# Kernel optimization log

Measured on AMD Instinct MI355X. Metric: run time of the kernel, lower is better.

## Reference

```python
import jax, jax.numpy as jnp
import numpy as np

N, S, R, CM = 1, 128, 256, 256
C, CZ = 32, 128


def setup_inputs() -> dict:
    key = jax.random.key(0)
    k1, k2, k3, k4 = jax.random.split(key, 4)
    return {
        "msa_repr": jax.random.normal(k1, (N, S, R, CM), dtype=jnp.float32),
        "left_proj": jax.random.normal(k2, (CM, C), dtype=jnp.float32) * 0.05,
        "right_proj": jax.random.normal(k3, (CM, C), dtype=jnp.float32) * 0.05,
        "out_proj": jax.random.normal(k4, (C * C, CZ), dtype=jnp.float32) * 0.05,
    }


def reference(msa_repr, left_proj, right_proj, out_proj):
    # msa_repr: [N, S, R, CM]
    # Project to left/right activations and move R before S
    # (equivalent to torch matmul + transpose(-2, -3)).
    a = jnp.einsum("nsrm,mc->nrsc", msa_repr, left_proj)   # [N, R, S, C]
    b = jnp.einsum("nsrm,mc->nrsc", msa_repr, right_proj)  # [N, R, S, C]
    # Outer product contracted over the MSA dim S:
    # outer[n, r, t, c, e] = sum_s a[n, r, s, c] * b[n, t, s, e]
    outer = jnp.einsum("nrsc,ntse->nrtce", a, b)            # [N, R, R, C, C]
    n, r, t = outer.shape[:3]
    outer = outer.reshape(n, r, t, C * C)                   # [N, R, R, C*C]
    # Output projection to pair channels cz
    return outer @ out_proj                                 # [N, R, R, CZ]
```

## Files before the change

### kernel.cpp

```cpp
#include <hip/hip_runtime.h>

typedef __bf16 bf16x8 __attribute__((ext_vector_type(8)));
typedef __bf16 bf16x4 __attribute__((ext_vector_type(4)));
typedef float f32x16 __attribute__((ext_vector_type(16)));
typedef float f32x4 __attribute__((ext_vector_type(4)));

constexpr int S = 128, R = 256, CM = 256, C = 32, CZ = 128;

#define MFMA __builtin_amdgcn_mfma_f32_32x32x16_bf16

__device__ __forceinline__ bf16x4 cvt4(float a, float b, float c, float d) {
    bf16x4 r;
    r[0] = (__bf16)a; r[1] = (__bf16)b; r[2] = (__bf16)c; r[3] = (__bf16)d;
    return r;
}

__global__ __launch_bounds__(256) void k_prep(const float* __restrict__ W,
                                              const float* __restrict__ Lp,
                                              const float* __restrict__ Rp,
                                              __bf16* __restrict__ WTf,
                                              __bf16* __restrict__ WLRT) {
    int b = blockIdx.x;
    if (b < 512) {
        int g = b * 256 + threadIdx.x;
        int cz = g & 127;
        int k = g >> 7;
        int e = k >> 5, c = k & 31;
        float v = W[(size_t)(c * 32 + e) * 128 + cz];
        WTf[((size_t)(k >> 3) * 128 + cz) * 8 + (k & 7)] = (__bf16)v;
    } else {
        int c = b - 512;
        int m = threadIdx.x;
        const float* src = (c < 32) ? Lp : Rp;
        WLRT[(size_t)c * 256 + m] = (__bf16)src[(size_t)m * 32 + (c & 31)];
    }
}

__global__ __launch_bounds__(256) void k_proj(const float* __restrict__ msa,
                                              const __bf16* __restrict__ WLRT,
                                              __bf16* __restrict__ aTf,
                                              __bf16* __restrict__ bTf) {
    __shared__ __align__(16) __bf16 As[32 * 256];
    __shared__ __align__(16) char Pp[2 * 4096];
    const int r = blockIdx.x;
    const int sq = blockIdx.y;
    const int t = threadIdx.x;

#pragma unroll
    for (int it = 0; it < 8; ++it) {
        int idx = it * 256 + t;
        int row = idx >> 6;
        int cg = idx & 63;
        float4 v = *(const float4*)&msa[((size_t)(sq * 32 + row) * R + r) * CM + cg * 4];
        bf16x4 h = cvt4(v.x, v.y, v.z, v.w);
        int P = (cg >> 1) ^ (row & 15);
        *(bf16x4*)((char*)As + row * 512 + P * 16 + (cg & 1) * 8) = h;
    }
    __syncthreads();

    const int w = t >> 6;
    const int l = t & 63;
    const int l31 = t & 31;
    const int kh = (t >> 5) & 1;
    const int sd = w & 1;
    const int ksh = w >> 1;

    f32x16 acc;
#pragma unroll
    for (int q = 0; q < 16; ++q) acc[q] = 0.f;

    const bf16x8* wb = (const bf16x8*)&WLRT[(size_t)(sd * 32 + l31) * 256 + 8 * kh];
    const char* arow = (const char*)As + l31 * 512;

    __builtin_amdgcn_s_setprio(1);
#pragma unroll
    for (int j = 0; j < 8; ++j) {
        int ks = ksh * 8 + j;
        int P = (2 * ks + kh) ^ (l31 & 15);
        bf16x8 af = *(const bf16x8*)(arow + P * 16);
        acc = MFMA(af, wb[2 * ks], acc, 0, 0, 0);
    }
    __builtin_amdgcn_s_setprio(0);

    char* pbase = Pp + (size_t)sd * 4096;
    if (ksh == 1) {
#pragma unroll
        for (int pc = 0; pc < 4; ++pc) {
            f32x4 v;
            v[0] = acc[4 * pc + 0]; v[1] = acc[4 * pc + 1];
            v[2] = acc[4 * pc + 2]; v[3] = acc[4 * pc + 3];
            *(f32x4*)(pbase + ((pc * 64) + l) * 16) = v;
        }
    }
    __syncthreads();
    if (ksh == 0) {
#pragma unroll
        for (int pc = 0; pc < 4; ++pc) {
            f32x4 v = *(const f32x4*)(pbase + ((pc * 64) + l) * 16);
            acc[4 * pc + 0] += v[0]; acc[4 * pc + 1] += v[1];
            acc[4 * pc + 2] += v[2]; acc[4 * pc + 3] += v[3];
        }
        __bf16* dst = sd ? bTf : aTf;
#pragma unroll
        for (int q = 0; q < 4; ++q) {
            size_t base = (size_t)r * 4096 + (size_t)(2 * sq + (q >> 1)) * 512 +
                          (size_t)(q & 1) * 256 + (size_t)l31 * 8 + 4 * kh;
            *(bf16x4*)&dst[base] = cvt4(acc[4 * q + 0], acc[4 * q + 1],
                                        acc[4 * q + 2], acc[4 * q + 3]);
        }
    }
}

__global__ __launch_bounds__(512, 2) void k_main(const __bf16* __restrict__ aTf,
                                                 const __bf16* __restrict__ bTf,
                                                 const __bf16* __restrict__ WTf,
                                                 float* __restrict__ out) {
    __shared__ __align__(16) __bf16 Gs[64 * 1024];

    const int t = threadIdx.x;
    const int w = t >> 6;
    const int l = t & 63;
    const int lane = l & 31;
    const int kh = l >> 5;
    const int r0 = blockIdx.x * 8;
    const int t0 = blockIdx.y * 8;

    const int rg = w & 3;
    const int tg = w >> 2;

    f32x16 acc[2][4];
#pragma unroll
    for (int i = 0; i < 2; ++i)
#pragma unroll
        for (int j = 0; j < 4; ++j)
#pragma unroll
            for (int q = 0; q < 16; ++q) acc[i][j][q] = 0.f;

    const bf16x8* ap0 = (const bf16x8*)aTf + ((size_t)(r0 + 2 * rg + 0) * 512 + kh * 32 + lane);
    const bf16x8* ap1 = (const bf16x8*)aTf + ((size_t)(r0 + 2 * rg + 1) * 512 + kh * 32 + lane);
    const bf16x8* bp0 = (const bf16x8*)bTf + ((size_t)(t0 + 4 * tg + 0) * 512 + kh * 32 + lane);
    const bf16x8* bp1 = (const bf16x8*)bTf + ((size_t)(t0 + 4 * tg + 1) * 512 + kh * 32 + lane);
    const bf16x8* bp2 = (const bf16x8*)bTf + ((size_t)(t0 + 4 * tg + 2) * 512 + kh * 32 + lane);
    const bf16x8* bp3 = (const bf16x8*)bTf + ((size_t)(t0 + 4 * tg + 3) * 512 + kh * 32 + lane);

    bf16x8 Ap[3][2], Bp[3][4];
#pragma unroll
    for (int s = 0; s < 3; ++s) {
        Ap[s][0] = ap0[s * 64]; Ap[s][1] = ap1[s * 64];
        Bp[s][0] = bp0[s * 64]; Bp[s][1] = bp1[s * 64];
        Bp[s][2] = bp2[s * 64]; Bp[s][3] = bp3[s * 64];
    }
#pragma unroll
    for (int ks = 0; ks < 8; ++ks) {
        const int s = ks % 3;
        __builtin_amdgcn_s_setprio(1);
        acc[0][0] = MFMA(Ap[s][0], Bp[s][0], acc[0][0], 0, 0, 0);
        acc[0][1] = MFMA(Ap[s][0], Bp[s][1], acc[0][1], 0, 0, 0);
        acc[0][2] = MFMA(Ap[s][0], Bp[s][2], acc[0][2], 0, 0, 0);
        acc[0][3] = MFMA(Ap[s][0], Bp[s][3], acc[0][3], 0, 0, 0);
        acc[1][0] = MFMA(Ap[s][1], Bp[s][0], acc[1][0], 0, 0, 0);
        acc[1][1] = MFMA(Ap[s][1], Bp[s][1], acc[1][1], 0, 0, 0);
        acc[1][2] = MFMA(Ap[s][1], Bp[s][2], acc[1][2], 0, 0, 0);
        acc[1][3] = MFMA(Ap[s][1], Bp[s][3], acc[1][3], 0, 0, 0);
        __builtin_amdgcn_s_setprio(0);
        if (ks + 3 < 8) {
            const int kn = ks + 3;
            Ap[s][0] = ap0[kn * 64]; Ap[s][1] = ap1[kn * 64];
            Bp[s][0] = bp0[kn * 64]; Bp[s][1] = bp1[kn * 64];
            Bp[s][2] = bp2[kn * 64]; Bp[s][3] = bp3[kn * 64];
        }
    }

#pragma unroll
    for (int i = 0; i < 2; ++i) {
#pragma unroll
        for (int j = 0; j < 4; ++j) {
            int p = (2 * rg + i) * 8 + 4 * tg + j;
            unsigned prow = (unsigned)p * 2048;
#pragma unroll
            for (int q = 0; q < 4; ++q) {
                int Lc = lane * 4 + q;
                int P = Lc ^ (p & 15) ^ (lane & 7);
                *(bf16x4*)((char*)Gs + prow + (unsigned)P * 16 + kh * 8) =
                    cvt4(acc[i][j][4 * q + 0], acc[i][j][4 * q + 1],
                         acc[i][j][4 * q + 2], acc[i][j][4 * q + 3]);
            }
        }
    }
    __syncthreads();

    const int kq = w >> 1;
    const int ng = w & 1;
    const int czl0 = ng * 64 + lane;
    const int czl1 = czl0 + 32;
    const char* wb0c = (const char*)WTf + ((size_t)kh * 128 + czl0) * 16;
    const char* wb1c = (const char*)WTf + ((size_t)kh * 128 + czl1) * 16;
    const unsigned prow0 = (unsigned)lane * 2048;
    const unsigned prow1 = (unsigned)(lane + 32) * 2048;
    const int p15 = lane & 15;

    f32x16 o00, o01, o10, o11;
#pragma unroll
    for (int q = 0; q < 16; ++q) { o00[q] = 0.f; o01[q] = 0.f; o10[q] = 0.f; o11[q] = 0.f; }

    bf16x8 Wp[16][2];
#pragma unroll
    for (int s = 0; s < 16; ++s) {
        const char* a0 = wb0c + (size_t)(kq * 16 + s) * 4096;
        const char* a1 = wb1c + (size_t)(kq * 16 + s) * 4096;
        asm volatile("global_load_dwordx4 %0, %1, off" : "=v"(Wp[s][0]) : "v"(a0));
        asm volatile("global_load_dwordx4 %0, %1, off" : "=v"(Wp[s][1]) : "v"(a1));
    }

    bf16x8 Gp[4][2];
#define LDG(sl, kk) do { \
    int Lr = (kk) * 2 + kh; \
    int P = Lr ^ p15 ^ ((Lr >> 2) & 7); \
    Gp[sl][0] = *(const bf16x8*)((const char*)Gs + prow0 + (unsigned)P * 16); \
    Gp[sl][1] = *(const bf16x8*)((const char*)Gs + prow1 + (unsigned)P * 16); } while (0)

    LDG(0, kq * 16 + 0);
    LDG(1, kq * 16 + 1);
    LDG(2, kq * 16 + 2);
    LDG(3, kq * 16 + 3);

#define STEPB(j, cnt) do { \
    asm volatile("s_waitcnt vmcnt(" #cnt ")"); \
    __builtin_amdgcn_sched_barrier(0); \
    __builtin_amdgcn_s_setprio(1); \
    o00 = MFMA(Gp[(j) & 3][0], Wp[j][0], o00, 0, 0, 0); \
    o01 = MFMA(Gp[(j) & 3][0], Wp[j][1], o01, 0, 0, 0); \
    o10 = MFMA(Gp[(j) & 3][1], Wp[j][0], o10, 0, 0, 0); \
    o11 = MFMA(Gp[(j) & 3][1], Wp[j][1], o11, 0, 0, 0); \
    __builtin_amdgcn_s_setprio(0); \
    if ((j) + 4 < 16) LDG((j) & 3, kq * 16 + (j) + 4); \
} while (0)

    STEPB(0, 30);  STEPB(1, 28);  STEPB(2, 26);  STEPB(3, 24);
    STEPB(4, 22);  STEPB(5, 20);  STEPB(6, 18);  STEPB(7, 16);
    STEPB(8, 14);  STEPB(9, 12);  STEPB(10, 10); STEPB(11, 8);
    STEPB(12, 6);  STEPB(13, 4);  STEPB(14, 2);  STEPB(15, 0);

    __syncthreads();

    {
        char* pr = (char*)Gs + (size_t)w * 16384;
        const f32x16* os[4] = {&o00, &o01, &o10, &o11};
#pragma unroll
        for (int s2 = 0; s2 < 4; ++s2) {
#pragma unroll
            for (int pc = 0; pc < 4; ++pc) {
                f32x4 v;
                v[0] = (*os[s2])[4 * pc + 0]; v[1] = (*os[s2])[4 * pc + 1];
                v[2] = (*os[s2])[4 * pc + 2]; v[3] = (*os[s2])[4 * pc + 3];
                *(f32x4*)(pr + ((s2 * 4 + pc) * 64 + l) * 16) = v;
            }
        }
    }
    __syncthreads();

    {
        const int ngx = w >> 2;
        const int mix = (w >> 1) & 1;
        const int nix = w & 1;
        const int s2 = mix * 2 + nix;
        f32x16 sm;
#pragma unroll
        for (int q = 0; q < 16; ++q) sm[q] = 0.f;
#pragma unroll
        for (int kq2 = 0; kq2 < 4; ++kq2) {
            const char* pr = (const char*)Gs + (size_t)(kq2 * 2 + ngx) * 16384;
#pragma unroll
            for (int pc = 0; pc < 4; ++pc) {
                f32x4 v = *(const f32x4*)(pr + ((s2 * 4 + pc) * 64 + l) * 16);
                sm[4 * pc + 0] += v[0]; sm[4 * pc + 1] += v[1];
                sm[4 * pc + 2] += v[2]; sm[4 * pc + 3] += v[3];
            }
        }
        const int czl = ngx * 64 + nix * 32 + (l & 31);
        const int khx = l >> 5;
#pragma unroll
        for (int reg = 0; reg < 16; ++reg) {
            int pl = mix * 32 + (reg & 3) + 8 * (reg >> 2) + 4 * khx;
            int prr = pl >> 3, ptt = pl & 7;
            out[((size_t)(r0 + prr) * 256 + (t0 + ptt)) * 128 + czl] = sm[reg];
        }
    }
}

extern "C" void kernel_launch(void* const* d_in, const int* in_sizes, int n_in,
                              void* d_out, int out_size, void* d_ws, size_t ws_size,
                              hipStream_t stream) {
    const float* msa = (const float*)d_in[0];
    const float* left = (const float*)d_in[1];
    const float* right = (const float*)d_in[2];
    const float* W = (const float*)d_in[3];

    __bf16* aTf = (__bf16*)d_ws;
    __bf16* bTf = aTf + (size_t)R * 4096;
    __bf16* WTf = bTf + (size_t)R * 4096;
    __bf16* WLRT = WTf + (size_t)128 * 1024;
    float* outp = (float*)d_out;

    k_prep<<<576, 256, 0, stream>>>(W, left, right, WTf, WLRT);
    k_proj<<<dim3(256, 4), 256, 0, stream>>>(msa, WLRT, aTf, bTf);
    k_main<<<dim3(32, 32), 512, 0, stream>>>(aTf, bTf, WTf, outp);
}
```

Baseline: 60.34 us.

## Stage a/b operand tiles into LDS via direct global_load_lds before MFMA loop

The per-wave global register loads of the a and b operand rows, with their 3-deep register prefetch, are replaced by a block-wide bulk copy of the block's 8 a-rows and 8 b-rows into shared memory using direct global-to-LDS loads. The MFMA loop then reads operands from LDS with double-buffered registers. This aims to issue all global traffic up front as wide coalesced transfers and overlap LDS reads with MFMAs. The trade-off is a full vmcnt wait plus barrier before any compute, and an extra barrier before the Gs buffer is reused for the G tile.

```diff
diff --git a/kernel.cpp b/kernel.cpp
--- a/kernel.cpp
+++ b/kernel.cpp
@@ -8,6 +8,9 @@
 constexpr int S = 128, R = 256, CM = 256, C = 32, CZ = 128;
 
 #define MFMA __builtin_amdgcn_mfma_f32_32x32x16_bf16
+
+typedef __attribute__((address_space(3))) void lds_void;
+typedef const __attribute__((address_space(1))) void gbl_void;
 
 __device__ __forceinline__ bf16x4 cvt4(float a, float b, float c, float d) {
     bf16x4 r;
@@ -125,6 +128,28 @@
     const int r0 = blockIdx.x * 8;
     const int t0 = blockIdx.y * 8;
 
+    {
+        const char* bsrc = (const char*)bTf + (size_t)t0 * 8192;
+        const char* asrc = (const char*)aTf + (size_t)r0 * 8192;
+        char* ldsb = (char*)Gs;
+        const unsigned wu = (unsigned)w * 1024;
+#pragma unroll
+        for (int i = 0; i < 8; ++i) {
+            __builtin_amdgcn_global_load_lds(
+                (gbl_void*)(bsrc + (size_t)i * 8192 + (size_t)t * 16),
+                (lds_void*)(ldsb + i * 8192 + wu), 16, 0, 0);
+        }
+#pragma unroll
+        for (int i = 0; i < 8; ++i) {
+            __builtin_amdgcn_global_load_lds(
+                (gbl_void*)(asrc + (size_t)i * 8192 + (size_t)t * 16),
+                (lds_void*)(ldsb + 65536 + i * 8192 + wu), 16, 0, 0);
+        }
+    }
+    asm volatile("s_waitcnt vmcnt(0)");
+    __builtin_amdgcn_sched_barrier(0);
+    __syncthreads();
+
     const int rg = w & 3;
     const int tg = w >> 2;
 
@@ -136,40 +161,42 @@
 #pragma unroll
             for (int q = 0; q < 16; ++q) acc[i][j][q] = 0.f;
 
-    const bf16x8* ap0 = (const bf16x8*)aTf + ((size_t)(r0 + 2 * rg + 0) * 512 + kh * 32 + lane);
-    const bf16x8* ap1 = (const bf16x8*)aTf + ((size_t)(r0 + 2 * rg + 1) * 512 + kh * 32 + lane);
-    const bf16x8* bp0 = (const bf16x8*)bTf + ((size_t)(t0 + 4 * tg + 0) * 512 + kh * 32 + lane);
-    const bf16x8* bp1 = (const bf16x8*)bTf + ((size_t)(t0 + 4 * tg + 1) * 512 + kh * 32 + lane);
-    const bf16x8* bp2 = (const bf16x8*)bTf + ((size_t)(t0 + 4 * tg + 2) * 512 + kh * 32 + lane);
-    const bf16x8* bp3 = (const bf16x8*)bTf + ((size_t)(t0 + 4 * tg + 3) * 512 + kh * 32 + lane);
-
-    bf16x8 Ap[3][2], Bp[3][4];
-#pragma unroll
-    for (int s = 0; s < 3; ++s) {
-        Ap[s][0] = ap0[s * 64]; Ap[s][1] = ap1[s * 64];
-        Bp[s][0] = bp0[s * 64]; Bp[s][1] = bp1[s * 64];
-        Bp[s][2] = bp2[s * 64]; Bp[s][3] = bp3[s * 64];
-    }
-#pragma unroll
-    for (int ks = 0; ks < 8; ++ks) {
-        const int s = ks % 3;
-        __builtin_amdgcn_s_setprio(1);
-        acc[0][0] = MFMA(Ap[s][0], Bp[s][0], acc[0][0], 0, 0, 0);
-        acc[0][1] = MFMA(Ap[s][0], Bp[s][1], acc[0][1], 0, 0, 0);
-        acc[0][2] = MFMA(Ap[s][0], Bp[s][2], acc[0][2], 0, 0, 0);
-        acc[0][3] = MFMA(Ap[s][0], Bp[s][3], acc[0][3], 0, 0, 0);
-        acc[1][0] = MFMA(Ap[s][1], Bp[s][0], acc[1][0], 0, 0, 0);
-        acc[1][1] = MFMA(Ap[s][1], Bp[s][1], acc[1][1], 0, 0, 0);
-        acc[1][2] = MFMA(Ap[s][1], Bp[s][2], acc[1][2], 0, 0, 0);
-        acc[1][3] = MFMA(Ap[s][1], Bp[s][3], acc[1][3], 0, 0, 0);
-        __builtin_amdgcn_s_setprio(0);
-        if (ks + 3 < 8) {
-            const int kn = ks + 3;
-            Ap[s][0] = ap0[kn * 64]; Ap[s][1] = ap1[kn * 64];
-            Bp[s][0] = bp0[kn * 64]; Bp[s][1] = bp1[kn * 64];
-            Bp[s][2] = bp2[kn * 64]; Bp[s][3] = bp3[kn * 64];
-        }
-    }
+    const char* aL0 = (const char*)Gs + 65536 + (2 * rg + 0) * 8192 + kh * 512 + lane * 16;
+    const char* aL1 = (const char*)Gs + 65536 + (2 * rg + 1) * 8192 + kh * 512 + lane * 16;
+    const char* bL0 = (const char*)Gs + (4 * tg + 0) * 8192 + kh * 512 + lane * 16;
+    const char* bL1 = (const char*)Gs + (4 * tg + 1) * 8192 + kh * 512 + lane * 16;
+    const char* bL2 = (const char*)Gs + (4 * tg + 2) * 8192 + kh * 512 + lane * 16;
+    const char* bL3 = (const char*)Gs + (4 * tg + 3) * 8192 + kh * 512 + lane * 16;
+
+    bf16x8 A0[2], B0[4], A1[2], B1[4];
+#define LDA(Aa, Bb, ks) do { \
+    Aa[0] = *(const bf16x8*)(aL0 + (ks) * 1024); \
+    Aa[1] = *(const bf16x8*)(aL1 + (ks) * 1024); \
+    Bb[0] = *(const bf16x8*)(bL0 + (ks) * 1024); \
+    Bb[1] = *(const bf16x8*)(bL1 + (ks) * 1024); \
+    Bb[2] = *(const bf16x8*)(bL2 + (ks) * 1024); \
+    Bb[3] = *(const bf16x8*)(bL3 + (ks) * 1024); } while (0)
+#define PH_A(Aa, Bb) do { \
+    __builtin_amdgcn_s_setprio(1); \
+    acc[0][0] = MFMA(Aa[0], Bb[0], acc[0][0], 0, 0, 0); \
+    acc[0][1] = MFMA(Aa[0], Bb[1], acc[0][1], 0, 0, 0); \
+    acc[0][2] = MFMA(Aa[0], Bb[2], acc[0][2], 0, 0, 0); \
+    acc[0][3] = MFMA(Aa[0], Bb[3], acc[0][3], 0, 0, 0); \
+    acc[1][0] = MFMA(Aa[1], Bb[0], acc[1][0], 0, 0, 0); \
+    acc[1][1] = MFMA(Aa[1], Bb[1], acc[1][1], 0, 0, 0); \
+    acc[1][2] = MFMA(Aa[1], Bb[2], acc[1][2], 0, 0, 0); \
+    acc[1][3] = MFMA(Aa[1], Bb[3], acc[1][3], 0, 0, 0); \
+    __builtin_amdgcn_s_setprio(0); } while (0)
+
+    LDA(A0, B0, 0);
+#pragma unroll
+    for (int ks = 0; ks < 8; ks += 2) {
+        LDA(A1, B1, ks + 1);
+        PH_A(A0, B0);
+        LDA(A0, B0, (ks + 2) & 7);
+        PH_A(A1, B1);
+    }
+    __syncthreads();
 
 #pragma unroll
     for (int i = 0; i < 2; ++i) {
```

After: 61.48 us. No clear change (+1.9%).
